# Kernel optimization log

Hardware: AMD Instinct MI355X
Metric: run time of the kernel (lower is better)

## Reference

```python
import jax, jax.numpy as jnp
import numpy as np

EPS_NORM = 1e-12
EPS_ABS = 1e-12


def _stack3(x):
    # x: [B, T, C] -> [B, T, 3, C] with left-shift, identity, right-shift taps
    prev = jnp.pad(x[:, :-1, :], ((0, 0), (1, 0), (0, 0)))
    nxt = jnp.pad(x[:, 1:, :], ((0, 0), (0, 1), (0, 0)))
    return jnp.stack([prev, x, nxt], axis=2)


def _l2_norm(x, axis):
    # matches layer's l2_normal: sqrt(max(sum(x^2), eps)), keepdims
    sq = jnp.sum(jnp.square(x), axis=axis, keepdims=True)
    return jnp.sqrt(jnp.maximum(sq, EPS_NORM))


def setup_inputs() -> dict:
    key = jax.random.key(0)
    k1, k2 = jax.random.split(key)
    B, T, C, K, U = 32, 4096, 128, 3, 256
    inputs = jax.random.normal(k1, (B, T, C), dtype=jnp.float32)
    # glorot uniform for w: limit = sqrt(6/(fan_in+fan_out)) with fan_in=C*K, fan_out=U
    limit = np.sqrt(6.0 / (C * K + U)).astype(np.float32)
    w = jax.random.uniform(k2, (1, C * K, U), dtype=jnp.float32, minval=-limit, maxval=limit)
    b = jnp.zeros((U,), dtype=jnp.float32)
    p = jnp.ones((U,), dtype=jnp.float32)
    q = jnp.zeros((1,), dtype=jnp.float32)
    return {"inputs": inputs, "w": w, "b": b, "p": p, "q": q}


def reference(inputs, w, b, p, q):
    B, T, C = inputs.shape
    U = w.shape[-1]
    x = _stack3(inputs).reshape(B, T, 3 * C)          # [B, T, 3C] (tap-major, matches tf stack+reshape)
    q2 = jnp.square(q)                                 # [1]
    x_norm = _l2_norm(x, axis=2) + q2                  # [B, T, 1]
    w_norm = _l2_norm(w, axis=1) + q2                  # [1, 1, U]
    w2 = w[0]                                          # [3C, U]
    sign = jnp.sign(jnp.einsum('btk,ku->btu', x, w2))  # sign of raw matmul
    y = jnp.einsum('btk,ku->btu', x / x_norm, w2 / w_norm[0])
    y = jnp.abs(y) + EPS_ABS
    y = jnp.power(y, jnp.square(p))                    # broadcast over units
    y = sign * y + b
    return y
```

## Files before the change

### kernel.cpp

```cpp
#include <hip/hip_runtime.h>

typedef __attribute__((ext_vector_type(8))) short short8;
typedef __attribute__((ext_vector_type(4))) float f32x4;

#define T_DIM 4096
#define C_DIM 128
#define U_DIM 256
#define BM 32
#define NROWS 34
#define LDK 136

__device__ __forceinline__ unsigned short f2bf(float f) {
    unsigned int u = __float_as_uint(f);
    u += 0x7FFFu + ((u >> 16) & 1u);
    return (unsigned short)(u >> 16);
}

__global__ void prep_kernel(const float* __restrict__ w,
                            const float* __restrict__ b,
                            const float* __restrict__ p,
                            const float* __restrict__ q,
                            unsigned short* __restrict__ wfrag,
                            float* __restrict__ winv,
                            float* __restrict__ p2,
                            float* __restrict__ bc) {
    if (blockIdx.x < 48) {
        int idx = blockIdx.x * 256 + threadIdx.x;
        int l  = idx & 63;
        int nt = (idx >> 6) & 15;
        int ks = idx >> 10;
        int n  = nt * 16 + (l & 15);
        int k0 = ks * 32 + ((l >> 4) << 3);
        #pragma unroll
        for (int j = 0; j < 8; ++j) {
            wfrag[(size_t)idx * 8 + j] = f2bf(w[(k0 + j) * U_DIM + n]);
        }
    } else {
        int u = threadIdx.x;
        float ss = 0.f;
        for (int k = 0; k < 3 * C_DIM; ++k) {
            float v = w[k * U_DIM + u];
            ss += v * v;
        }
        float q2 = q[0] * q[0];
        winv[u] = 1.0f / (sqrtf(fmaxf(ss, 1e-12f)) + q2);
        float pv = p[u];
        p2[u] = pv * pv;
        bc[u] = b[u];
    }
}

__global__ __launch_bounds__(256, 4) void cossim_main(
        const float* __restrict__ inp,
        const unsigned short* __restrict__ wfrag,
        const float* __restrict__ winv,
        const float* __restrict__ p2g,
        const float* __restrict__ bg,
        const float* __restrict__ qg,
        float* __restrict__ out) {
    __shared__ unsigned short inp_s[NROWS][LDK];
    __shared__ float ss_s[NROWS];

    const int tid  = threadIdx.x;
    const int bidx = blockIdx.x;
    const int bb   = bidx >> 7;
    const int t0   = (bidx & 127) * BM;

    {
        const int r0 = tid >> 5;
        const int lc = (tid & 31) * 4;
        float4 v[5];
        #pragma unroll
        for (int i = 0; i < 5; ++i) {
            int r = r0 + i * 8;
            int t = t0 + r - 1;
            float4 val = make_float4(0.f, 0.f, 0.f, 0.f);
            if (r < NROWS && (unsigned)t < T_DIM)
                val = *(const float4*)(inp + ((size_t)bb * T_DIM + t) * C_DIM + lc);
            v[i] = val;
        }
        #pragma unroll
        for (int i = 0; i < 5; ++i) {
            int r = r0 + i * 8;
            if (r < NROWS) {
                float4 val = v[i];
                float part = val.x * val.x + val.y * val.y + val.z * val.z + val.w * val.w;
                #pragma unroll
                for (int o = 16; o > 0; o >>= 1) part += __shfl_xor(part, o, 32);
                if ((tid & 31) == 0) ss_s[r] = part;
                ushort4 sv;
                sv.x = f2bf(val.x); sv.y = f2bf(val.y);
                sv.z = f2bf(val.z); sv.w = f2bf(val.w);
                *(ushort4*)(&inp_s[r][lc]) = sv;
            }
        }
    }
    __syncthreads();

    const int uw  = tid >> 6;
    const int l   = tid & 63;
    const int l15 = l & 15;
    const int lg  = l >> 4;

    f32x4 acc[2][4];
    #pragma unroll
    for (int tf = 0; tf < 2; ++tf)
        #pragma unroll
        for (int uf = 0; uf < 4; ++uf)
            acc[tf][uf] = (f32x4){0.f, 0.f, 0.f, 0.f};

    const short8* wf = (const short8*)wfrag;

    #pragma unroll
    for (int ks = 0; ks < 12; ++ks) {
        const int tap = ks >> 2;
        const int c0  = (ks & 3) * 32 + lg * 8;
        short8 xv[2], wv[4];
        #pragma unroll
        for (int tf = 0; tf < 2; ++tf) {
            int row = tf * 16 + l15 + tap;
            xv[tf] = *(const short8*)(&inp_s[row][c0]);
        }
        #pragma unroll
        for (int uf = 0; uf < 4; ++uf) {
            wv[uf] = wf[(size_t)(ks * 16 + uw * 4 + uf) * 64 + l];
        }
        #pragma unroll
        for (int tf = 0; tf < 2; ++tf)
            #pragma unroll
            for (int uf = 0; uf < 4; ++uf)
                acc[tf][uf] = __builtin_amdgcn_mfma_f32_16x16x32_bf16(
                    wv[uf], xv[tf], acc[tf][uf], 0, 0, 0);
    }

    const float q2 = qg[0] * qg[0];
    #pragma unroll
    for (int tf = 0; tf < 2; ++tf) {
        int trow = tf * 16 + l15;
        float s3 = ss_s[trow] + ss_s[trow + 1] + ss_s[trow + 2];
        float xi = 1.0f / (sqrtf(fmaxf(s3, 1e-12f)) + q2);
        float* orow = out + ((size_t)bb * T_DIM + t0 + trow) * U_DIM;
        #pragma unroll
        for (int uf = 0; uf < 4; ++uf) {
            int uc = uw * 64 + uf * 16 + lg * 4;
            f32x4 wiv = *(const f32x4*)(winv + uc);
            f32x4 ppv = *(const f32x4*)(p2g + uc);
            f32x4 bbv = *(const f32x4*)(bg + uc);
            f32x4 r;
            #pragma unroll
            for (int j = 0; j < 4; ++j) {
                float raw = acc[tf][uf][j];
                float y   = raw * xi * wiv[j];
                float ay  = fabsf(y) + 1e-12f;
                float pw  = ppv[j];
                float rr  = ay;
                if (pw != 1.0f) rr = powf(ay, pw);
                float s   = (raw > 0.f) ? 1.f : ((raw < 0.f) ? -1.f : 0.f);
                r[j] = s * rr + bbv[j];
            }
            *(f32x4*)(orow + uc) = r;
        }
    }
}

extern "C" void kernel_launch(void* const* d_in, const int* in_sizes, int n_in,
                              void* d_out, int out_size, void* d_ws, size_t ws_size,
                              hipStream_t stream) {
    const float* inp = (const float*)d_in[0];
    const float* w   = (const float*)d_in[1];
    const float* b   = (const float*)d_in[2];
    const float* p   = (const float*)d_in[3];
    const float* q   = (const float*)d_in[4];
    float* out = (float*)d_out;

    unsigned short* wfrag = (unsigned short*)d_ws;
    float* winv = (float*)((char*)d_ws + 196608);
    float* p2   = winv + 256;
    float* bc   = p2 + 256;

    prep_kernel<<<49, 256, 0, stream>>>(w, b, p, q, wfrag, winv, p2, bc);
    cossim_main<<<4096, 256, 0, stream>>>(inp, wfrag, winv, p2, bc, q, out);
}
```

Before: 78.86 us.

## Split each tile into four single-wave blocks with remapped block order

The block is cut from four waves to one wave of 64 threads. Each block now computes one quarter of the output units for a 32-row tile, so the grid grows fourfold. Block IDs are remapped so that the four unit-quarters of a tile are spread apart, presumably to balance work across XCDs or share the input through L2. The cost is that each input tile is loaded and converted to bf16 four times instead of once. The row norm inverse is precomputed once into shared memory.

```diff
diff --git a/kernel.cpp b/kernel.cpp
--- a/kernel.cpp
+++ b/kernel.cpp
@@ -7,7 +7,7 @@
 #define C_DIM 128
 #define U_DIM 256
 #define BM 32
-#define NROWS 34
+#define NRW 34
 #define LDK 136
 
 __device__ __forceinline__ unsigned short f2bf(float f) {
@@ -50,7 +50,7 @@
     }
 }
 
-__global__ __launch_bounds__(256, 4) void cossim_main(
+__global__ __launch_bounds__(64, 4) void cossim_main(
         const float* __restrict__ inp,
         const unsigned short* __restrict__ wfrag,
         const float* __restrict__ winv,
@@ -58,49 +58,49 @@
         const float* __restrict__ bg,
         const float* __restrict__ qg,
         float* __restrict__ out) {
-    __shared__ unsigned short inp_s[NROWS][LDK];
-    __shared__ float ss_s[NROWS];
+    __shared__ unsigned short xs[NRW][LDK];
+    __shared__ float ss_s[NRW];
+    __shared__ float xninv_s[BM];
 
-    const int tid  = threadIdx.x;
-    const int bidx = blockIdx.x;
-    const int bb   = bidx >> 7;
-    const int t0   = (bidx & 127) * BM;
+    const int tid = threadIdx.x;
+
+    int bid = blockIdx.x;
+    bid = (bid & 7) * 2048 + (bid >> 3);
+    const int bb = bid >> 9;
+    const int tt = (bid >> 2) & 127;
+    const int uq = bid & 3;
+    const int t0 = tt * BM;
+
+    const float q2 = qg[0] * qg[0];
 
     {
-        const int r0 = tid >> 5;
-        const int lc = (tid & 31) * 4;
-        float4 v[5];
-        #pragma unroll
-        for (int i = 0; i < 5; ++i) {
-            int r = r0 + i * 8;
+        const int half = tid >> 5;
+        const int lc   = (tid & 31) * 4;
+        for (int rr = 0; rr < 17; ++rr) {
+            int r = rr * 2 + half;
             int t = t0 + r - 1;
-            float4 val = make_float4(0.f, 0.f, 0.f, 0.f);
-            if (r < NROWS && (unsigned)t < T_DIM)
-                val = *(const float4*)(inp + ((size_t)bb * T_DIM + t) * C_DIM + lc);
-            v[i] = val;
-        }
-        #pragma unroll
-        for (int i = 0; i < 5; ++i) {
-            int r = r0 + i * 8;
-            if (r < NROWS) {
-                float4 val = v[i];
-                float part = val.x * val.x + val.y * val.y + val.z * val.z + val.w * val.w;
-                #pragma unroll
-                for (int o = 16; o > 0; o >>= 1) part += __shfl_xor(part, o, 32);
-                if ((tid & 31) == 0) ss_s[r] = part;
-                ushort4 sv;
-                sv.x = f2bf(val.x); sv.y = f2bf(val.y);
-                sv.z = f2bf(val.z); sv.w = f2bf(val.w);
-                *(ushort4*)(&inp_s[r][lc]) = sv;
-            }
+            float4 v = make_float4(0.f, 0.f, 0.f, 0.f);
+            if ((unsigned)t < T_DIM)
+                v = *(const float4*)(inp + ((size_t)bb * T_DIM + t) * C_DIM + lc);
+            float part = v.x * v.x + v.y * v.y + v.z * v.z + v.w * v.w;
+            #pragma unroll
+            for (int o = 16; o > 0; o >>= 1) part += __shfl_xor(part, o, 32);
+            if ((tid & 31) == 0) ss_s[r] = part;
+            ushort4 sv;
+            sv.x = f2bf(v.x); sv.y = f2bf(v.y);
+            sv.z = f2bf(v.z); sv.w = f2bf(v.w);
+            *(ushort4*)(&xs[r][lc]) = sv;
         }
     }
     __syncthreads();
+    if (tid < BM) {
+        float s3 = ss_s[tid] + ss_s[tid + 1] + ss_s[tid + 2];
+        xninv_s[tid] = 1.0f / (sqrtf(fmaxf(s3, 1e-12f)) + q2);
+    }
+    __syncthreads();
 
-    const int uw  = tid >> 6;
-    const int l   = tid & 63;
-    const int l15 = l & 15;
-    const int lg  = l >> 4;
+    const int l15 = tid & 15;
+    const int lg  = tid >> 4;
 
     f32x4 acc[2][4];
     #pragma unroll
@@ -119,12 +119,11 @@
         #pragma unroll
         for (int tf = 0; tf < 2; ++tf) {
             int row = tf * 16 + l15 + tap;
-            xv[tf] = *(const short8*)(&inp_s[row][c0]);
+            xv[tf] = *(const short8*)(&xs[row][c0]);
         }
         #pragma unroll
-        for (int uf = 0; uf < 4; ++uf) {
-            wv[uf] = wf[(size_t)(ks * 16 + uw * 4 + uf) * 64 + l];
-        }
+        for (int uf = 0; uf < 4; ++uf)
+            wv[uf] = wf[(size_t)(ks * 16 + uq * 4 + uf) * 64 + tid];
         #pragma unroll
         for (int tf = 0; tf < 2; ++tf)
             #pragma unroll
@@ -133,16 +132,14 @@
                     wv[uf], xv[tf], acc[tf][uf], 0, 0, 0);
     }
 
-    const float q2 = qg[0] * qg[0];
     #pragma unroll
     for (int tf = 0; tf < 2; ++tf) {
         int trow = tf * 16 + l15;
-        float s3 = ss_s[trow] + ss_s[trow + 1] + ss_s[trow + 2];
-        float xi = 1.0f / (sqrtf(fmaxf(s3, 1e-12f)) + q2);
+        float xi = xninv_s[trow];
         float* orow = out + ((size_t)bb * T_DIM + t0 + trow) * U_DIM;
         #pragma unroll
         for (int uf = 0; uf < 4; ++uf) {
-            int uc = uw * 64 + uf * 16 + lg * 4;
+            int uc = uq * 64 + uf * 16 + lg * 4;
             f32x4 wiv = *(const f32x4*)(winv + uc);
             f32x4 ppv = *(const f32x4*)(p2g + uc);
             f32x4 bbv = *(const f32x4*)(bg + uc);
@@ -179,5 +176,5 @@
     float* bc   = p2 + 256;
 
     prep_kernel<<<49, 256, 0, stream>>>(w, b, p, q, wfrag, winv, p2, bc);
-    cossim_main<<<4096, 256, 0, stream>>>(inp, wfrag, winv, p2, bc, q, out);
+    cossim_main<<<16384, 64, 0, stream>>>(inp, wfrag, winv, p2, bc, q, out);
 }
```

Result: slower. 96.90 us (+22.9%).
